# Performance work log

Hardware: AMD Instinct MI355X
Metric: run time of the kernel (lower is better)

The kernel has to match this reference:

```python
import jax, jax.numpy as jnp
import numpy as np

E = 8        # num_experts
TOPK = 2     # k
D = 1024     # input/output size
H = 4096     # expert hidden size


def setup_inputs() -> dict:
    key = jax.random.key(0)
    ks = jax.random.split(key, 8)
    s = 0.02
    return {
        "hidden_states": jax.random.normal(ks[0], (2, 2048, D), dtype=jnp.float32),
        "Wr": jax.random.normal(ks[1], (D, E), dtype=jnp.float32) * s,
        "br": jnp.zeros((E,), dtype=jnp.float32),
        "gate_bias": jnp.zeros((E,), dtype=jnp.float32),
        "W1": jax.random.normal(ks[2], (E, D, H), dtype=jnp.float32) * s,
        "b1": jnp.zeros((E, H), dtype=jnp.float32),
        "W2": jax.random.normal(ks[3], (E, H, D), dtype=jnp.float32) * s,
        "b2": jnp.zeros((E, D), dtype=jnp.float32),
    }


def reference(hidden_states, Wr, br, gate_bias, W1, b1, W2, b2):
    B, S, Din = hidden_states.shape
    x = hidden_states.reshape(B * S, Din)              # [T, D]
    # Router: logits + gate bias, top-k, softmax over the k selected logits
    logits = x @ Wr + br + gate_bias                   # [T, E]
    top_v, top_i = jax.lax.top_k(logits, TOPK)         # [T, k]
    probs = jax.nn.softmax(top_v, axis=-1)             # [T, k]
    # Scatter top-k probs into dense per-expert gate weights [T, E]
    gate = jnp.einsum("tk,tke->te", probs,
                      jax.nn.one_hot(top_i, E, dtype=probs.dtype))
    # Per-expert MLP (exact gelu, eval mode -> no dropout/noise),
    # weighted-combine; zero gate weight == token not routed to expert.
    out = jnp.zeros((B * S, W2.shape[-1]), dtype=x.dtype)
    for e in range(E):
        h = jax.nn.gelu(x @ W1[e] + b1[e], approximate=False)  # [T, H]
        y = h @ W2[e] + b2[e]                                  # [T, D]
        out = out + gate[:, e:e + 1] * y
    return out.reshape(B, S, -1)
```

## Files before the change

kernel.cpp:

```cpp
#include <hip/hip_runtime.h>
#include <hip/hip_bf16.h>
#include <stdint.h>
#include <stddef.h>


#define T_TOK 4096
#define DIM   1024
#define HID   4096
#define NE    8

typedef unsigned short u16;
typedef __bf16 bf16x8 __attribute__((ext_vector_type(8)));
typedef float  f32x4  __attribute__((ext_vector_type(4)));
typedef u16    u16x8  __attribute__((ext_vector_type(8)));

__device__ __forceinline__ u16 f2bf(float f) {
  union { float f; uint32_t u; } v; v.f = f;
  uint32_t u = v.u;
  return (u16)((u + 0x7fffu + ((u >> 16) & 1u)) >> 16);
}

__device__ __forceinline__ void async_load16(const void* g, void* l) {
  typedef __attribute__((address_space(1))) void GPtr;
  typedef __attribute__((address_space(3))) void LPtr;
  __builtin_amdgcn_global_load_lds((GPtr*)g, (LPtr*)l, 16, 0, 0);
}

__global__ void router_kernel(const float* __restrict__ x, const float* __restrict__ Wr,
                              const float* __restrict__ br, const float* __restrict__ gb,
                              int* __restrict__ counts, int* __restrict__ lists,
                              float* __restrict__ gate_p) {
  const int t = blockIdx.x * 4 + (threadIdx.x >> 6);
  const int lane = threadIdx.x & 63;
  const float* xr = x + (size_t)t * DIM;
  float acc[NE];
#pragma unroll
  for (int e = 0; e < NE; ++e) acc[e] = 0.f;
#pragma unroll
  for (int i = 0; i < DIM / 64; ++i) {
    const int k = i * 64 + lane;
    const float xv = xr[k];
    const float4 w0 = *reinterpret_cast<const float4*>(Wr + (size_t)k * NE);
    const float4 w1 = *reinterpret_cast<const float4*>(Wr + (size_t)k * NE + 4);
    acc[0] += xv * w0.x; acc[1] += xv * w0.y; acc[2] += xv * w0.z; acc[3] += xv * w0.w;
    acc[4] += xv * w1.x; acc[5] += xv * w1.y; acc[6] += xv * w1.z; acc[7] += xv * w1.w;
  }
#pragma unroll
  for (int off = 32; off >= 1; off >>= 1) {
#pragma unroll
    for (int e = 0; e < NE; ++e) acc[e] += __shfl_xor(acc[e], off);
  }
  if (lane == 0) {
    float lg[NE];
#pragma unroll
    for (int e = 0; e < NE; ++e) lg[e] = acc[e] + br[e] + gb[e];
    int i0 = 0;
#pragma unroll
    for (int e = 1; e < NE; ++e) if (lg[e] > lg[i0]) i0 = e;
    int i1 = (i0 == 0) ? 1 : 0;
#pragma unroll
    for (int e = 0; e < NE; ++e) if (e != i0 && lg[e] > lg[i1]) i1 = e;
    const float ev = expf(lg[i1] - lg[i0]);
    const float p0 = 1.f / (1.f + ev);
    const float p1 = ev / (1.f + ev);
    const int pos0 = atomicAdd(&counts[i0], 1);
    lists[i0 * T_TOK + pos0] = t * 2 + 0;
    const int pos1 = atomicAdd(&counts[i1], 1);
    lists[i1 * T_TOK + pos1] = t * 2 + 1;
    gate_p[t * 2 + 0] = p0;
    gate_p[t * 2 + 1] = p1;
  }
}

__global__ void cvt_x_kernel(const float* __restrict__ in, u16* __restrict__ out, int n8) {
  const int i = blockIdx.x * blockDim.x + threadIdx.x;
  if (i >= n8) return;
  const float4 a = reinterpret_cast<const float4*>(in)[2 * i];
  const float4 b = reinterpret_cast<const float4*>(in)[2 * i + 1];
  u16x8 r;
  r[0] = f2bf(a.x); r[1] = f2bf(a.y); r[2] = f2bf(a.z); r[3] = f2bf(a.w);
  r[4] = f2bf(b.x); r[5] = f2bf(b.y); r[6] = f2bf(b.z); r[7] = f2bf(b.w);
  *reinterpret_cast<u16x8*>(out + (size_t)i * 8) = r;
}

__global__ void cvt_w_kernel(const float* __restrict__ in, u16* __restrict__ out,
                             int K, int N) {
  __shared__ float tile[64][65];
  const int e = blockIdx.z;
  const int n0 = blockIdx.x * 64, k0 = blockIdx.y * 64;
  const int tid = threadIdx.x;
  const float* src = in + (size_t)e * K * N;
#pragma unroll
  for (int r = 0; r < 16; ++r) {
    const int kr = r * 4 + (tid >> 6);
    tile[kr][tid & 63] = src[(size_t)(k0 + kr) * N + n0 + (tid & 63)];
  }
  __syncthreads();
  u16* dst = out + (size_t)e * N * K;
#pragma unroll
  for (int r = 0; r < 8; ++r) {
    const int nr = r * 8 + (tid >> 5);
    const int kc = (tid & 31) * 2;
    ushort2 v;
    v.x = f2bf(tile[kc][nr]);
    v.y = f2bf(tile[kc + 1][nr]);
    *reinterpret_cast<ushort2*>(&dst[(size_t)(n0 + nr) * K + k0 + kc]) = v;
  }
}

template <int KT, int NT, int PHASE>
__global__ __launch_bounds__(256, 2)
void gemm_kernel(const u16* __restrict__ Abase, const u16* __restrict__ Bt,
                 const float* __restrict__ bias, const int* __restrict__ counts,
                 const int* __restrict__ lists, const float* __restrict__ gate_p,
                 u16* __restrict__ hout, float* __restrict__ yout) {
  const int e = blockIdx.z;
  const int cnt = counts[e];
  const int m0 = blockIdx.y * 128;
  if (m0 >= cnt) return;
  const int n0 = blockIdx.x * 128;
  const int tid = threadIdx.x;
  const int lane = tid & 63, wid = tid >> 6;
  const int wr = wid >> 1, wc = wid & 1;

  __shared__ alignas(16) u16 As[128 * 72];
  __shared__ alignas(16) u16 Bs[128 * 64];
  __shared__ int rowp[128];

  if (tid < 128) {
    const int idx = m0 + tid;
    rowp[tid] = lists[e * T_TOK + (idx < cnt ? idx : cnt - 1)];
  }
  __syncthreads();

  const u16* aptr[4];
#pragma unroll
  for (int i = 0; i < 4; ++i) {
    const int r = i * 32 + (tid >> 3);
    const int p = rowp[r];
    const int arow = (PHASE == 1) ? (p >> 1) : p;
    aptr[i] = Abase + (size_t)arow * KT + (tid & 7) * 8;
  }
  const u16* bsrc = Bt + ((size_t)e * NT + n0) * KT;

  f32x4 acc[4][4];
#pragma unroll
  for (int a = 0; a < 4; ++a)
#pragma unroll
    for (int b = 0; b < 4; ++b) acc[a][b] = f32x4{0.f, 0.f, 0.f, 0.f};

  for (int k0 = 0; k0 < KT; k0 += 64) {
#pragma unroll
    for (int j = 0; j < 4; ++j) {
      const int brow = j * 32 + wid * 8;
      const u16* src = bsrc + (size_t)(brow + (lane >> 3)) * KT + k0 + (lane & 7) * 8;
      async_load16(src, &Bs[brow * 64]);
    }
#pragma unroll
    for (int i = 0; i < 4; ++i) {
      const bf16x8 v = *reinterpret_cast<const bf16x8*>(aptr[i] + k0);
      *reinterpret_cast<bf16x8*>(&As[((size_t)(i * 32 + (tid >> 3))) * 72 + (tid & 7) * 8]) = v;
    }
    __syncthreads();
#pragma unroll
    for (int kk = 0; kk < 2; ++kk) {
      bf16x8 af[4], bfr[4];
#pragma unroll
      for (int fm = 0; fm < 4; ++fm)
        af[fm] = *reinterpret_cast<const bf16x8*>(
            &As[(wr * 64 + fm * 16 + (lane & 15)) * 72 + kk * 32 + (lane >> 4) * 8]);
#pragma unroll
      for (int fn = 0; fn < 4; ++fn)
        bfr[fn] = *reinterpret_cast<const bf16x8*>(
            &Bs[(wc * 64 + fn * 16 + (lane & 15)) * 64 + kk * 32 + (lane >> 4) * 8]);
#pragma unroll
      for (int fm = 0; fm < 4; ++fm)
#pragma unroll
        for (int fn = 0; fn < 4; ++fn)
          acc[fm][fn] = __builtin_amdgcn_mfma_f32_16x16x32_bf16(af[fm], bfr[fn],
                                                                acc[fm][fn], 0, 0, 0);
    }
    __syncthreads();
  }

  const float* bias_e = bias + (size_t)e * NT;
#pragma unroll
  for (int fm = 0; fm < 4; ++fm) {
#pragma unroll
    for (int r = 0; r < 4; ++r) {
      const int row = wr * 64 + fm * 16 + (lane >> 4) * 4 + r;
      if (m0 + row >= cnt) continue;
      const int p = rowp[row];
#pragma unroll
      for (int fn = 0; fn < 4; ++fn) {
        const int n = n0 + wc * 64 + fn * 16 + (lane & 15);
        const float v = acc[fm][fn][r] + bias_e[n];
        if (PHASE == 1) {
          const float g = 0.5f * v * (1.0f + erff(v * 0.70710678118654752f));
          hout[(size_t)p * NT + n] = f2bf(g);
        } else if (PHASE == 2) {
          yout[(size_t)p * NT + n] = gate_p[p] * v;
        } else {
          atomicAdd(&yout[(size_t)(p >> 1) * NT + n], gate_p[p] * v);
        }
      }
    }
  }
}

__global__ void combine_kernel(const float* __restrict__ yp, float* __restrict__ out) {
  const int i = blockIdx.x * blockDim.x + threadIdx.x;
  const int t = i >> 8;
  const int d4 = i & 255;
  const float4 a = reinterpret_cast<const float4*>(yp)[(size_t)(2 * t) * 256 + d4];
  const float4 b = reinterpret_cast<const float4*>(yp)[(size_t)(2 * t) * 256 + 256 + d4];
  float4 o; o.x = a.x + b.x; o.y = a.y + b.y; o.z = a.z + b.z; o.w = a.w + b.w;
  reinterpret_cast<float4*>(out)[i] = o;
}

extern "C" void kernel_launch(void* const* d_in, const int* in_sizes, int n_in,
                              void* d_out, int out_size, void* d_ws, size_t ws_size,
                              hipStream_t stream) {
  const float* x  = (const float*)d_in[0];
  const float* Wr = (const float*)d_in[1];
  const float* br = (const float*)d_in[2];
  const float* gb = (const float*)d_in[3];
  const float* W1 = (const float*)d_in[4];
  const float* b1 = (const float*)d_in[5];
  const float* W2 = (const float*)d_in[6];
  const float* b2 = (const float*)d_in[7];
  float* out = (float*)d_out;

  char* ws = (char*)d_ws;
  size_t off = 0;
  int*   counts = (int*)(ws + off);   off += 256;
  int*   lists  = (int*)(ws + off);   off += (size_t)NE * T_TOK * 4;
  float* gate_p = (float*)(ws + off); off += (size_t)T_TOK * 2 * 4;
  u16*   xb     = (u16*)(ws + off);   off += (size_t)T_TOK * DIM * 2;
  u16*   wbuf   = (u16*)(ws + off);   off += (size_t)NE * DIM * HID * 2;
  u16*   hbuf   = (u16*)(ws + off);   off += (size_t)T_TOK * 2 * HID * 2;
  const size_t need_base = off;
  float* ypair  = (float*)(ws + off);
  const size_t need_full = off + (size_t)T_TOK * 2 * DIM * 4;
  const bool use_ypair = (ws_size >= need_full);
  (void)need_base;

  hipMemsetAsync(counts, 0, 32, stream);
  router_kernel<<<T_TOK / 4, 256, 0, stream>>>(x, Wr, br, gb, counts, lists, gate_p);
  cvt_x_kernel<<<(T_TOK * DIM / 8 + 255) / 256, 256, 0, stream>>>(x, xb, T_TOK * DIM / 8);
  cvt_w_kernel<<<dim3(HID / 64, DIM / 64, NE), 256, 0, stream>>>(W1, wbuf, DIM, HID);
  gemm_kernel<DIM, HID, 1><<<dim3(HID / 128, T_TOK / 128, NE), 256, 0, stream>>>(
      xb, wbuf, b1, counts, lists, gate_p, hbuf, nullptr);
  cvt_w_kernel<<<dim3(DIM / 64, HID / 64, NE), 256, 0, stream>>>(W2, wbuf, HID, DIM);
  if (use_ypair) {
    gemm_kernel<HID, DIM, 2><<<dim3(DIM / 128, T_TOK / 128, NE), 256, 0, stream>>>(
        hbuf, wbuf, b2, counts, lists, gate_p, nullptr, ypair);
    combine_kernel<<<T_TOK, 256, 0, stream>>>(ypair, out);
  } else {
    hipMemsetAsync(out, 0, (size_t)out_size * 4, stream);
    gemm_kernel<HID, DIM, 3><<<dim3(DIM / 128, T_TOK / 128, NE), 256, 0, stream>>>(
        hbuf, wbuf, b2, counts, lists, gate_p, nullptr, out);
  }
}
```

Measured before the change: 476.6 us.

## Double-buffer GEMM LDS tiles with prefetch and XOR-swizzle B layout

The expert GEMM kernel now keeps two LDS buffers for the A and B tiles. While MFMAs run on the current tile, it prefetches the next K tile: A goes through registers and B through async global-to-LDS loads. This needs one barrier per step instead of two. B tiles are also stored with an XOR swizzle of their 16-byte slots to cut LDS bank conflicts on the fragment reads. The cost is doubled LDS use (about 69KB per block), which may limit occupancy against the launch bound of 2 blocks per CU, plus extra register pressure from the prefetch.

```diff
diff --git a/kernel.cpp b/kernel.cpp
--- a/kernel.cpp
+++ b/kernel.cpp
@@ -123,8 +123,8 @@
   const int lane = tid & 63, wid = tid >> 6;
   const int wr = wid >> 1, wc = wid & 1;
 
-  __shared__ alignas(16) u16 As[128 * 72];
-  __shared__ alignas(16) u16 Bs[128 * 64];
+  __shared__ alignas(16) u16 As[2][128 * 72];
+  __shared__ alignas(16) u16 Bs[2][128 * 64];
   __shared__ int rowp[128];
 
   if (tid < 128) {
@@ -142,6 +142,8 @@
     aptr[i] = Abase + (size_t)arow * KT + (tid & 7) * 8;
   }
   const u16* bsrc = Bt + ((size_t)e * NT + n0) * KT;
+  const int brow_lane = lane >> 3;
+  const int bslot = (lane & 7) ^ brow_lane;
 
   f32x4 acc[4][4];
 #pragma unroll
@@ -149,39 +151,73 @@
 #pragma unroll
     for (int b = 0; b < 4; ++b) acc[a][b] = f32x4{0.f, 0.f, 0.f, 0.f};
 
-  for (int k0 = 0; k0 < KT; k0 += 64) {
-#pragma unroll
-    for (int j = 0; j < 4; ++j) {
-      const int brow = j * 32 + wid * 8;
-      const u16* src = bsrc + (size_t)(brow + (lane >> 3)) * KT + k0 + (lane & 7) * 8;
-      async_load16(src, &Bs[brow * 64]);
-    }
-#pragma unroll
-    for (int i = 0; i < 4; ++i) {
-      const bf16x8 v = *reinterpret_cast<const bf16x8*>(aptr[i] + k0);
-      *reinterpret_cast<bf16x8*>(&As[((size_t)(i * 32 + (tid >> 3))) * 72 + (tid & 7) * 8]) = v;
-    }
-    __syncthreads();
-#pragma unroll
-    for (int kk = 0; kk < 2; ++kk) {
-      bf16x8 af[4], bfr[4];
-#pragma unroll
-      for (int fm = 0; fm < 4; ++fm)
-        af[fm] = *reinterpret_cast<const bf16x8*>(
-            &As[(wr * 64 + fm * 16 + (lane & 15)) * 72 + kk * 32 + (lane >> 4) * 8]);
-#pragma unroll
-      for (int fn = 0; fn < 4; ++fn)
-        bfr[fn] = *reinterpret_cast<const bf16x8*>(
-            &Bs[(wc * 64 + fn * 16 + (lane & 15)) * 64 + kk * 32 + (lane >> 4) * 8]);
-#pragma unroll
-      for (int fm = 0; fm < 4; ++fm)
-#pragma unroll
-        for (int fn = 0; fn < 4; ++fn)
-          acc[fm][fn] = __builtin_amdgcn_mfma_f32_16x16x32_bf16(af[fm], bfr[fn],
-                                                                acc[fm][fn], 0, 0, 0);
-    }
-    __syncthreads();
-  }
+  constexpr int nkt = KT / 64;
+  bf16x8 areg[4];
+
+#pragma unroll
+  for (int i = 0; i < 4; ++i) areg[i] = *reinterpret_cast<const bf16x8*>(aptr[i]);
+#pragma unroll
+  for (int j = 0; j < 4; ++j) {
+    const int brow = j * 32 + wid * 8;
+    async_load16(bsrc + (size_t)(brow + brow_lane) * KT + bslot * 8, &Bs[0][brow * 64]);
+  }
+#pragma unroll
+  for (int i = 0; i < 4; ++i)
+    *reinterpret_cast<bf16x8*>(&As[0][(i * 32 + (tid >> 3)) * 72 + (tid & 7) * 8]) = areg[i];
+  __syncthreads();
+
+#define GEMM_STEP(CUR, NXT, T)                                                       \
+  {                                                                                  \
+    const int t_ = (T);                                                              \
+    const bool pf_ = (t_ + 1 < nkt);                                                 \
+    if (pf_) {                                                                       \
+      _Pragma("unroll")                                                              \
+      for (int i = 0; i < 4; ++i)                                                    \
+        areg[i] = *reinterpret_cast<const bf16x8*>(aptr[i] + (t_ + 1) * 64);         \
+      _Pragma("unroll")                                                              \
+      for (int j = 0; j < 4; ++j) {                                                  \
+        const int brow = j * 32 + wid * 8;                                           \
+        async_load16(bsrc + (size_t)(brow + brow_lane) * KT + (t_ + 1) * 64 +        \
+                         bslot * 8,                                                  \
+                     &Bs[NXT][brow * 64]);                                           \
+      }                                                                              \
+    }                                                                                \
+    _Pragma("unroll")                                                                \
+    for (int kk = 0; kk < 2; ++kk) {                                                 \
+      bf16x8 af[4], bfr[4];                                                          \
+      _Pragma("unroll")                                                              \
+      for (int fm = 0; fm < 4; ++fm)                                                 \
+        af[fm] = *reinterpret_cast<const bf16x8*>(                                   \
+            &As[CUR][(wr * 64 + fm * 16 + (lane & 15)) * 72 + kk * 32 +              \
+                     (lane >> 4) * 8]);                                              \
+      _Pragma("unroll")                                                              \
+      for (int fn = 0; fn < 4; ++fn) {                                               \
+        const int r2 = wc * 64 + fn * 16 + (lane & 15);                              \
+        const int ls = kk * 4 + (lane >> 4);                                         \
+        bfr[fn] = *reinterpret_cast<const bf16x8*>(                                  \
+            &Bs[CUR][r2 * 64 + ((ls ^ (r2 & 7)) * 8)]);                              \
+      }                                                                              \
+      _Pragma("unroll")                                                              \
+      for (int fm = 0; fm < 4; ++fm)                                                 \
+        _Pragma("unroll")                                                            \
+        for (int fn = 0; fn < 4; ++fn)                                               \
+          acc[fm][fn] = __builtin_amdgcn_mfma_f32_16x16x32_bf16(af[fm], bfr[fn],     \
+                                                                acc[fm][fn], 0, 0, 0); \
+    }                                                                                \
+    if (pf_) {                                                                       \
+      _Pragma("unroll")                                                              \
+      for (int i = 0; i < 4; ++i)                                                    \
+        *reinterpret_cast<bf16x8*>(                                                  \
+            &As[NXT][(i * 32 + (tid >> 3)) * 72 + (tid & 7) * 8]) = areg[i];         \
+    }                                                                                \
+    __syncthreads();                                                                 \
+  }
+
+  for (int t = 0; t < nkt; t += 2) {
+    GEMM_STEP(0, 1, t);
+    GEMM_STEP(1, 0, t + 1);
+  }
+#undef GEMM_STEP
 
   const float* bias_e = bias + (size_t)e * NT;
 #pragma unroll
@@ -239,11 +275,9 @@
   u16*   xb     = (u16*)(ws + off);   off += (size_t)T_TOK * DIM * 2;
   u16*   wbuf   = (u16*)(ws + off);   off += (size_t)NE * DIM * HID * 2;
   u16*   hbuf   = (u16*)(ws + off);   off += (size_t)T_TOK * 2 * HID * 2;
-  const size_t need_base = off;
   float* ypair  = (float*)(ws + off);
   const size_t need_full = off + (size_t)T_TOK * 2 * DIM * 4;
   const bool use_ypair = (ws_size >= need_full);
-  (void)need_base;
 
   hipMemsetAsync(counts, 0, 32, stream);
   router_kernel<<<T_TOK / 4, 256, 0, stream>>>(x, Wr, br, gb, counts, lists, gate_p);
```

Result: slower. 496.6 us (+4.2%).

## Rework expert GEMM into 256x128 tiles with triple-buffered async LDS pipeline

Applied to the files above, without the earlier changes.

Rewrites the grouped expert GEMM to use 512-thread blocks computing 256x128 output tiles, with both A (gathered token rows) and B loaded via async global-to-LDS copies into a three-stage ring buffer with XOR-swizzled layout. MFMA work is split into two halves per K step, with prefetch of stage t+2 issued between them and s_setprio raised around MFMA bursts. This aims to hide global-load latency and LDS bank conflicts and raise arithmetic intensity per block. It uses 144KB of LDS per block, which limits occupancy, and relies on hand-placed waitcnt and barriers being correct.

```diff
diff --git a/kernel.cpp b/kernel.cpp
--- a/kernel.cpp
+++ b/kernel.cpp
@@ -109,92 +109,160 @@
 }
 
 template <int KT, int NT, int PHASE>
-__global__ __launch_bounds__(256, 2)
+__global__ __launch_bounds__(512, 2)
 void gemm_kernel(const u16* __restrict__ Abase, const u16* __restrict__ Bt,
                  const float* __restrict__ bias, const int* __restrict__ counts,
                  const int* __restrict__ lists, const float* __restrict__ gate_p,
                  u16* __restrict__ hout, float* __restrict__ yout) {
   const int e = blockIdx.z;
   const int cnt = counts[e];
-  const int m0 = blockIdx.y * 128;
+  const int m0 = blockIdx.y * 256;
   if (m0 >= cnt) return;
   const int n0 = blockIdx.x * 128;
   const int tid = threadIdx.x;
-  const int lane = tid & 63, wid = tid >> 6;
-  const int wr = wid >> 1, wc = wid & 1;
-
-  __shared__ alignas(16) u16 As[128 * 72];
-  __shared__ alignas(16) u16 Bs[128 * 64];
-  __shared__ int rowp[128];
-
-  if (tid < 128) {
+  const int lane = tid & 63, w = tid >> 6;
+  const int wm = w >> 2, wn = w & 3;
+
+  __shared__ alignas(16) u16 lds[73728];
+  __shared__ int rowp[256];
+
+  if (tid < 256) {
     const int idx = m0 + tid;
     rowp[tid] = lists[e * T_TOK + (idx < cnt ? idx : cnt - 1)];
   }
   __syncthreads();
 
-  const u16* aptr[4];
+  const int srow = w * 8 + (lane >> 3);
+  const int sslot = (lane & 7) ^ (lane >> 3);
+  const u16* aP[4];
 #pragma unroll
   for (int i = 0; i < 4; ++i) {
-    const int r = i * 32 + (tid >> 3);
-    const int p = rowp[r];
+    const int p = rowp[i * 64 + srow];
     const int arow = (PHASE == 1) ? (p >> 1) : p;
-    aptr[i] = Abase + (size_t)arow * KT + (tid & 7) * 8;
-  }
-  const u16* bsrc = Bt + ((size_t)e * NT + n0) * KT;
-
-  f32x4 acc[4][4];
-#pragma unroll
-  for (int a = 0; a < 4; ++a)
-#pragma unroll
-    for (int b = 0; b < 4; ++b) acc[a][b] = f32x4{0.f, 0.f, 0.f, 0.f};
-
-  for (int k0 = 0; k0 < KT; k0 += 64) {
-#pragma unroll
-    for (int j = 0; j < 4; ++j) {
-      const int brow = j * 32 + wid * 8;
-      const u16* src = bsrc + (size_t)(brow + (lane >> 3)) * KT + k0 + (lane & 7) * 8;
-      async_load16(src, &Bs[brow * 64]);
+    aP[i] = Abase + (size_t)arow * KT + sslot * 8;
+  }
+  const u16* bP[2];
+#pragma unroll
+  for (int i = 0; i < 2; ++i)
+    bP[i] = Bt + ((size_t)e * NT + n0 + i * 64 + srow) * KT + sslot * 8;
+
+  constexpr int nkt = KT / 64;
+
+#define STAGE(TT, BB)                                                          \
+  {                                                                            \
+    _Pragma("unroll")                                                          \
+    for (int i = 0; i < 4; ++i)                                                \
+      async_load16(aP[i] + (TT) * 64, &lds[(BB) * 16384 + (i * 64 + w * 8) * 64]); \
+    _Pragma("unroll")                                                          \
+    for (int i = 0; i < 2; ++i)                                                \
+      async_load16(bP[i] + (TT) * 64,                                          \
+                   &lds[49152 + (BB) * 8192 + (i * 64 + w * 8) * 64]);         \
+  }
+
+  f32x4 acc[8][2];
+#pragma unroll
+  for (int a = 0; a < 8; ++a)
+#pragma unroll
+    for (int b = 0; b < 2; ++b) acc[a][b] = f32x4{0.f, 0.f, 0.f, 0.f};
+
+  STAGE(0, 0);
+  STAGE(1, 1);
+  asm volatile("s_waitcnt vmcnt(6)" ::: "memory");
+  __builtin_amdgcn_sched_barrier(0);
+  __builtin_amdgcn_s_barrier();
+
+  int cur = 0;
+  const int l15 = lane & 15, lks = lane >> 4;
+  for (int t = 0; t < nkt; ++t) {
+    const int abase = cur * 16384;
+    const int bbase = 49152 + cur * 8192;
+    bf16x8 bf[2][2];
+    {
+      bf16x8 af[4][2];
+#pragma unroll
+      for (int fm = 0; fm < 4; ++fm) {
+        const int r = wm * 128 + fm * 16 + l15;
+#pragma unroll
+        for (int ks = 0; ks < 2; ++ks) {
+          const int ls = ks * 4 + lks;
+          af[fm][ks] = *reinterpret_cast<const bf16x8*>(
+              &lds[abase + r * 64 + ((ls ^ (r & 7)) * 8)]);
+        }
+      }
+#pragma unroll
+      for (int nf = 0; nf < 2; ++nf) {
+        const int r = wn * 32 + nf * 16 + l15;
+#pragma unroll
+        for (int ks = 0; ks < 2; ++ks) {
+          const int ls = ks * 4 + lks;
+          bf[nf][ks] = *reinterpret_cast<const bf16x8*>(
+              &lds[bbase + r * 64 + ((ls ^ (r & 7)) * 8)]);
+        }
+      }
+      if (t + 2 < nkt) {
+        const int nxt2 = (cur == 0) ? 2 : cur - 1;
+        STAGE(t + 2, nxt2);
+      }
+      __builtin_amdgcn_s_barrier();
+      __builtin_amdgcn_s_setprio(1);
+#pragma unroll
+      for (int fm = 0; fm < 4; ++fm)
+#pragma unroll
+        for (int nf = 0; nf < 2; ++nf)
+#pragma unroll
+          for (int ks = 0; ks < 2; ++ks)
+            acc[fm][nf] = __builtin_amdgcn_mfma_f32_16x16x32_bf16(
+                af[fm][ks], bf[nf][ks], acc[fm][nf], 0, 0, 0);
+      __builtin_amdgcn_s_setprio(0);
+      __builtin_amdgcn_s_barrier();
     }
-#pragma unroll
-    for (int i = 0; i < 4; ++i) {
-      const bf16x8 v = *reinterpret_cast<const bf16x8*>(aptr[i] + k0);
-      *reinterpret_cast<bf16x8*>(&As[((size_t)(i * 32 + (tid >> 3))) * 72 + (tid & 7) * 8]) = v;
+    {
+      bf16x8 af[4][2];
+#pragma unroll
+      for (int fm = 0; fm < 4; ++fm) {
+        const int r = wm * 128 + 64 + fm * 16 + l15;
+#pragma unroll
+        for (int ks = 0; ks < 2; ++ks) {
+          const int ls = ks * 4 + lks;
+          af[fm][ks] = *reinterpret_cast<const bf16x8*>(
+              &lds[abase + r * 64 + ((ls ^ (r & 7)) * 8)]);
+        }
+      }
+      if (t < nkt - 2) {
+        asm volatile("s_waitcnt vmcnt(6)" ::: "memory");
+      } else if (t == nkt - 2) {
+        asm volatile("s_waitcnt vmcnt(0)" ::: "memory");
+      }
+      __builtin_amdgcn_sched_barrier(0);
+      __builtin_amdgcn_s_barrier();
+      __builtin_amdgcn_s_setprio(1);
+#pragma unroll
+      for (int fm = 0; fm < 4; ++fm)
+#pragma unroll
+        for (int nf = 0; nf < 2; ++nf)
+#pragma unroll
+          for (int ks = 0; ks < 2; ++ks)
+            acc[4 + fm][nf] = __builtin_amdgcn_mfma_f32_16x16x32_bf16(
+                af[fm][ks], bf[nf][ks], acc[4 + fm][nf], 0, 0, 0);
+      __builtin_amdgcn_s_setprio(0);
+      __builtin_amdgcn_s_barrier();
     }
-    __syncthreads();
-#pragma unroll
-    for (int kk = 0; kk < 2; ++kk) {
-      bf16x8 af[4], bfr[4];
-#pragma unroll
-      for (int fm = 0; fm < 4; ++fm)
-        af[fm] = *reinterpret_cast<const bf16x8*>(
-            &As[(wr * 64 + fm * 16 + (lane & 15)) * 72 + kk * 32 + (lane >> 4) * 8]);
-#pragma unroll
-      for (int fn = 0; fn < 4; ++fn)
-        bfr[fn] = *reinterpret_cast<const bf16x8*>(
-            &Bs[(wc * 64 + fn * 16 + (lane & 15)) * 64 + kk * 32 + (lane >> 4) * 8]);
-#pragma unroll
-      for (int fm = 0; fm < 4; ++fm)
-#pragma unroll
-        for (int fn = 0; fn < 4; ++fn)
-          acc[fm][fn] = __builtin_amdgcn_mfma_f32_16x16x32_bf16(af[fm], bfr[fn],
-                                                                acc[fm][fn], 0, 0, 0);
-    }
-    __syncthreads();
-  }
+    cur = (cur == 2) ? 0 : cur + 1;
+  }
+#undef STAGE
 
   const float* bias_e = bias + (size_t)e * NT;
 #pragma unroll
-  for (int fm = 0; fm < 4; ++fm) {
+  for (int fm = 0; fm < 8; ++fm) {
 #pragma unroll
     for (int r = 0; r < 4; ++r) {
-      const int row = wr * 64 + fm * 16 + (lane >> 4) * 4 + r;
+      const int row = wm * 128 + ((fm & 4) << 4) + (fm & 3) * 16 + (lane >> 4) * 4 + r;
       if (m0 + row >= cnt) continue;
       const int p = rowp[row];
 #pragma unroll
-      for (int fn = 0; fn < 4; ++fn) {
-        const int n = n0 + wc * 64 + fn * 16 + (lane & 15);
-        const float v = acc[fm][fn][r] + bias_e[n];
+      for (int nf = 0; nf < 2; ++nf) {
+        const int n = n0 + wn * 32 + nf * 16 + (lane & 15);
+        const float v = acc[fm][nf][r] + bias_e[n];
         if (PHASE == 1) {
           const float g = 0.5f * v * (1.0f + erff(v * 0.70710678118654752f));
           hout[(size_t)p * NT + n] = f2bf(g);
@@ -239,26 +307,24 @@
   u16*   xb     = (u16*)(ws + off);   off += (size_t)T_TOK * DIM * 2;
   u16*   wbuf   = (u16*)(ws + off);   off += (size_t)NE * DIM * HID * 2;
   u16*   hbuf   = (u16*)(ws + off);   off += (size_t)T_TOK * 2 * HID * 2;
-  const size_t need_base = off;
   float* ypair  = (float*)(ws + off);
   const size_t need_full = off + (size_t)T_TOK * 2 * DIM * 4;
   const bool use_ypair = (ws_size >= need_full);
-  (void)need_base;
 
   hipMemsetAsync(counts, 0, 32, stream);
   router_kernel<<<T_TOK / 4, 256, 0, stream>>>(x, Wr, br, gb, counts, lists, gate_p);
   cvt_x_kernel<<<(T_TOK * DIM / 8 + 255) / 256, 256, 0, stream>>>(x, xb, T_TOK * DIM / 8);
   cvt_w_kernel<<<dim3(HID / 64, DIM / 64, NE), 256, 0, stream>>>(W1, wbuf, DIM, HID);
-  gemm_kernel<DIM, HID, 1><<<dim3(HID / 128, T_TOK / 128, NE), 256, 0, stream>>>(
+  gemm_kernel<DIM, HID, 1><<<dim3(HID / 128, T_TOK * 2 / 256, NE), 512, 0, stream>>>(
       xb, wbuf, b1, counts, lists, gate_p, hbuf, nullptr);
   cvt_w_kernel<<<dim3(DIM / 64, HID / 64, NE), 256, 0, stream>>>(W2, wbuf, HID, DIM);
   if (use_ypair) {
-    gemm_kernel<HID, DIM, 2><<<dim3(DIM / 128, T_TOK / 128, NE), 256, 0, stream>>>(
+    gemm_kernel<HID, DIM, 2><<<dim3(DIM / 128, T_TOK * 2 / 256, NE), 512, 0, stream>>>(
         hbuf, wbuf, b2, counts, lists, gate_p, nullptr, ypair);
     combine_kernel<<<T_TOK, 256, 0, stream>>>(ypair, out);
   } else {
     hipMemsetAsync(out, 0, (size_t)out_size * 4, stream);
-    gemm_kernel<HID, DIM, 3><<<dim3(DIM / 128, T_TOK / 128, NE), 256, 0, stream>>>(
+    gemm_kernel<HID, DIM, 3><<<dim3(DIM / 128, T_TOK * 2 / 256, NE), 512, 0, stream>>>(
         hbuf, wbuf, b2, counts, lists, gate_p, nullptr, out);
   }
 }
```

After: 563.7 us. 1.18x slower.

## Rewrite MoE GEMM with 256x256 tiles, swizzled LDS pipeline, split-K and tile table

Applied to the files above, without the earlier changes.

The expert GEMM is restructured. It now uses 512-thread blocks computing 256x256 output tiles, XOR-swizzled LDS and a register-staged double buffer. Global loads for the next K step are interleaved with MFMA work across four barrier phases, and MFMA priority is raised. A small tile-table kernel packs only the occupied (expert, row-tile) pairs into the grid, replacing the dense expert × max-tile grid with its early exits. The second GEMM is split along K into two partial outputs, which a 4-way combine kernel sums. The aim is more data reuse per LDS load and better overlap of loads with MFMA, at the cost of a large 128KB LDS footprint (low occupancy) and extra partial-sum traffic.

```diff
diff --git a/kernel.cpp b/kernel.cpp
--- a/kernel.cpp
+++ b/kernel.cpp
@@ -8,6 +8,7 @@
 #define DIM   1024
 #define HID   4096
 #define NE    8
+#define MT_MAX 40
 
 typedef unsigned short u16;
 typedef __bf16 bf16x8 __attribute__((ext_vector_type(8)));
@@ -18,12 +19,6 @@
   union { float f; uint32_t u; } v; v.f = f;
   uint32_t u = v.u;
   return (u16)((u + 0x7fffu + ((u >> 16) & 1u)) >> 16);
-}
-
-__device__ __forceinline__ void async_load16(const void* g, void* l) {
-  typedef __attribute__((address_space(1))) void GPtr;
-  typedef __attribute__((address_space(3))) void LPtr;
-  __builtin_amdgcn_global_load_lds((GPtr*)g, (LPtr*)l, 16, 0, 0);
 }
 
 __global__ void router_kernel(const float* __restrict__ x, const float* __restrict__ Wr,
@@ -72,6 +67,20 @@
   }
 }
 
+__global__ void tile_table_kernel(const int* __restrict__ counts, int* __restrict__ tab) {
+  if (threadIdx.x == 0) {
+    int tot = 0;
+    for (int e = 0; e < NE; ++e) {
+      const int c = counts[e];
+      const int nt = (c + 255) >> 8;
+      for (int i = 0; i < nt && tot < MT_MAX; ++i) {
+        tab[tot * 2] = e; tab[tot * 2 + 1] = i * 256; ++tot;
+      }
+    }
+    for (; tot < MT_MAX; ++tot) tab[tot * 2] = -1;
+  }
+}
+
 __global__ void cvt_x_kernel(const float* __restrict__ in, u16* __restrict__ out, int n8) {
   const int i = blockIdx.x * blockDim.x + threadIdx.x;
   if (i >= n8) return;
@@ -108,113 +117,209 @@
   }
 }
 
-template <int KT, int NT, int PHASE>
-__global__ __launch_bounds__(256, 2)
+__device__ __forceinline__ void ld_afrags(const u16* sm, int cA, int fmh, int wm,
+                                          int l15, int swz0, int swz1, bf16x8 af[4][2]) {
+#pragma unroll
+  for (int f = 0; f < 4; ++f) {
+    const int r = fmh * 128 + wm * 64 + f * 16 + l15;
+    af[f][0] = *reinterpret_cast<const bf16x8*>(&sm[cA + r * 64 + swz0 * 8]);
+    af[f][1] = *reinterpret_cast<const bf16x8*>(&sm[cA + r * 64 + swz1 * 8]);
+  }
+}
+__device__ __forceinline__ void ld_bfrags(const u16* sm, int cA, int nfh, int wn,
+                                          int l15, int swz0, int swz1, bf16x8 bfr[2][2]) {
+#pragma unroll
+  for (int g = 0; g < 2; ++g) {
+    const int r = nfh * 128 + wn * 32 + g * 16 + l15;
+    bfr[g][0] = *reinterpret_cast<const bf16x8*>(&sm[32768 + cA + r * 64 + swz0 * 8]);
+    bfr[g][1] = *reinterpret_cast<const bf16x8*>(&sm[32768 + cA + r * 64 + swz1 * 8]);
+  }
+}
+__device__ __forceinline__ void wr_half(u16* sm, int baseoff, int h, int trow, int wslot,
+                                        const bf16x8 v[2]) {
+#pragma unroll
+  for (int j = 0; j < 2; ++j) {
+    const int r = h * 128 + j * 64 + trow;
+    *reinterpret_cast<bf16x8*>(&sm[baseoff + r * 64 + wslot * 8]) = v[j];
+  }
+}
+
+#define PH_SYNC()                                           \
+  asm volatile("s_waitcnt lgkmcnt(0)" ::: "memory");        \
+  __builtin_amdgcn_s_barrier();                             \
+  __builtin_amdgcn_sched_barrier(0);
+
+#define MMQ(FMH, NFH, AF, BF)                                                   \
+  __builtin_amdgcn_s_setprio(1);                                                \
+  _Pragma("unroll") for (int f_ = 0; f_ < 4; ++f_)                              \
+  _Pragma("unroll") for (int g_ = 0; g_ < 2; ++g_)                              \
+  _Pragma("unroll") for (int ks_ = 0; ks_ < 2; ++ks_)                           \
+    acc[(FMH) * 4 + f_][(NFH) * 2 + g_] =                                       \
+        __builtin_amdgcn_mfma_f32_16x16x32_bf16(                                \
+            AF[f_][ks_], BF[g_][ks_], acc[(FMH) * 4 + f_][(NFH) * 2 + g_],      \
+            0, 0, 0);                                                           \
+  __builtin_amdgcn_s_setprio(0);
+
+template <int KT, int NT, int NSPLIT, int PHASE>
+__global__ __launch_bounds__(512, 2)
 void gemm_kernel(const u16* __restrict__ Abase, const u16* __restrict__ Bt,
                  const float* __restrict__ bias, const int* __restrict__ counts,
                  const int* __restrict__ lists, const float* __restrict__ gate_p,
+                 const int* __restrict__ tab,
                  u16* __restrict__ hout, float* __restrict__ yout) {
-  const int e = blockIdx.z;
+  const int e = tab[blockIdx.x * 2];
+  if (e < 0) return;
+  const int m0 = tab[blockIdx.x * 2 + 1];
   const int cnt = counts[e];
-  const int m0 = blockIdx.y * 128;
-  if (m0 >= cnt) return;
-  const int n0 = blockIdx.x * 128;
+  const int n0 = blockIdx.y * 256;
+  const int z = blockIdx.z;
+  const int kbase = z * (KT / NSPLIT);
+  constexpr int nkt = (KT / NSPLIT) / 64;
+
   const int tid = threadIdx.x;
-  const int lane = tid & 63, wid = tid >> 6;
-  const int wr = wid >> 1, wc = wid & 1;
-
-  __shared__ alignas(16) u16 As[128 * 72];
-  __shared__ alignas(16) u16 Bs[128 * 64];
-  __shared__ int rowp[128];
-
-  if (tid < 128) {
+  const int lane = tid & 63, w = tid >> 6;
+  const int wm = w >> 2, wn = w & 3;
+  const int l15 = lane & 15, lks = lane >> 4;
+  const int rb = l15 & 7;
+  const int swz0 = lks ^ rb, swz1 = (4 + lks) ^ rb;
+
+  __shared__ alignas(16) u16 lds[65536];
+  __shared__ int rowp[256];
+
+  if (tid < 256) {
     const int idx = m0 + tid;
     rowp[tid] = lists[e * T_TOK + (idx < cnt ? idx : cnt - 1)];
   }
   __syncthreads();
 
-  const u16* aptr[4];
-#pragma unroll
-  for (int i = 0; i < 4; ++i) {
-    const int r = i * 32 + (tid >> 3);
-    const int p = rowp[r];
-    const int arow = (PHASE == 1) ? (p >> 1) : p;
-    aptr[i] = Abase + (size_t)arow * KT + (tid & 7) * 8;
-  }
-  const u16* bsrc = Bt + ((size_t)e * NT + n0) * KT;
-
-  f32x4 acc[4][4];
-#pragma unroll
-  for (int a = 0; a < 4; ++a)
+  const int trow = tid >> 3;
+  const int tslot = tid & 7;
+  const int wslot = tslot ^ (trow & 7);
+  const u16* aP[2][2];
+  const u16* bP[2][2];
+#pragma unroll
+  for (int h = 0; h < 2; ++h)
+#pragma unroll
+    for (int j = 0; j < 2; ++j) {
+      const int r = h * 128 + j * 64 + trow;
+      const int p = rowp[r];
+      const int arow = (PHASE == 1) ? (p >> 1) : p;
+      aP[h][j] = Abase + (size_t)arow * KT + kbase + tslot * 8;
+      bP[h][j] = Bt + ((size_t)e * NT + n0 + r) * KT + kbase + tslot * 8;
+    }
+
+  f32x4 acc[8][4];
+#pragma unroll
+  for (int a = 0; a < 8; ++a)
 #pragma unroll
     for (int b = 0; b < 4; ++b) acc[a][b] = f32x4{0.f, 0.f, 0.f, 0.f};
 
-  for (int k0 = 0; k0 < KT; k0 += 64) {
-#pragma unroll
-    for (int j = 0; j < 4; ++j) {
-      const int brow = j * 32 + wid * 8;
-      const u16* src = bsrc + (size_t)(brow + (lane >> 3)) * KT + k0 + (lane & 7) * 8;
-      async_load16(src, &Bs[brow * 64]);
+  bf16x8 aL0[2], aL1[2], bL0[2], bL1[2], af[4][2], bfr[2][2];
+
+  {
+    bf16x8 w0[2], w1[2];
+#pragma unroll
+    for (int j = 0; j < 2; ++j) {
+      w0[j]  = *reinterpret_cast<const bf16x8*>(aP[0][j]);
+      w1[j]  = *reinterpret_cast<const bf16x8*>(bP[0][j]);
+      aL1[j] = *reinterpret_cast<const bf16x8*>(aP[1][j]);
+      bL1[j] = *reinterpret_cast<const bf16x8*>(bP[1][j]);
     }
-#pragma unroll
-    for (int i = 0; i < 4; ++i) {
-      const bf16x8 v = *reinterpret_cast<const bf16x8*>(aptr[i] + k0);
-      *reinterpret_cast<bf16x8*>(&As[((size_t)(i * 32 + (tid >> 3))) * 72 + (tid & 7) * 8]) = v;
-    }
-    __syncthreads();
-#pragma unroll
-    for (int kk = 0; kk < 2; ++kk) {
-      bf16x8 af[4], bfr[4];
-#pragma unroll
-      for (int fm = 0; fm < 4; ++fm)
-        af[fm] = *reinterpret_cast<const bf16x8*>(
-            &As[(wr * 64 + fm * 16 + (lane & 15)) * 72 + kk * 32 + (lane >> 4) * 8]);
-#pragma unroll
-      for (int fn = 0; fn < 4; ++fn)
-        bfr[fn] = *reinterpret_cast<const bf16x8*>(
-            &Bs[(wc * 64 + fn * 16 + (lane & 15)) * 64 + kk * 32 + (lane >> 4) * 8]);
-#pragma unroll
-      for (int fm = 0; fm < 4; ++fm)
-#pragma unroll
-        for (int fn = 0; fn < 4; ++fn)
-          acc[fm][fn] = __builtin_amdgcn_mfma_f32_16x16x32_bf16(af[fm], bfr[fn],
-                                                                acc[fm][fn], 0, 0, 0);
-    }
-    __syncthreads();
-  }
+    wr_half(lds, 0, 0, trow, wslot, w0);
+    wr_half(lds, 32768, 0, trow, wslot, w1);
+  }
+
+#define TILE(C, T)                                                                   \
+  {                                                                                  \
+    constexpr int cA = (C) * 16384;                                                  \
+    constexpr int nA = ((C) ^ 1) * 16384;                                            \
+    const int tn = (T) + 1;                                                          \
+                                       \
+    PH_SYNC();                                                                       \
+    ld_afrags(lds, cA, 0, wm, l15, swz0, swz1, af);                                  \
+    ld_bfrags(lds, cA, 0, wn, l15, swz0, swz1, bfr);                                 \
+    if (tn < nkt) {                                                                  \
+      aL0[0] = *reinterpret_cast<const bf16x8*>(aP[0][0] + tn * 64);                 \
+      aL0[1] = *reinterpret_cast<const bf16x8*>(aP[0][1] + tn * 64);                 \
+    }                                                                                \
+    wr_half(lds, 32768 + cA, 1, trow, wslot, bL1);                                   \
+    MMQ(0, 0, af, bfr);                                                              \
+                                          \
+    PH_SYNC();                                                                       \
+    ld_bfrags(lds, cA, 1, wn, l15, swz0, swz1, bfr);                                 \
+    if (tn < nkt) {                                                                  \
+      bL0[0] = *reinterpret_cast<const bf16x8*>(bP[0][0] + tn * 64);                 \
+      bL0[1] = *reinterpret_cast<const bf16x8*>(bP[0][1] + tn * 64);                 \
+    }                                                                                \
+    wr_half(lds, cA, 1, trow, wslot, aL1);                                           \
+    MMQ(0, 1, af, bfr);                                                              \
+                                      \
+    PH_SYNC();                                                                       \
+    ld_afrags(lds, cA, 1, wm, l15, swz0, swz1, af);                                  \
+    ld_bfrags(lds, cA, 0, wn, l15, swz0, swz1, bfr);                                 \
+    if (tn < nkt) {                                                                  \
+      bL1[0] = *reinterpret_cast<const bf16x8*>(bP[1][0] + tn * 64);                 \
+      bL1[1] = *reinterpret_cast<const bf16x8*>(bP[1][1] + tn * 64);                 \
+    }                                                                                \
+    wr_half(lds, nA, 0, trow, wslot, aL0);                                           \
+    MMQ(1, 0, af, bfr);                                                              \
+                            \
+    ld_bfrags(lds, cA, 1, wn, l15, swz0, swz1, bfr);                                 \
+    if (tn < nkt) {                                                                  \
+      aL1[0] = *reinterpret_cast<const bf16x8*>(aP[1][0] + tn * 64);                 \
+      aL1[1] = *reinterpret_cast<const bf16x8*>(aP[1][1] + tn * 64);                 \
+    }                                                                                \
+    wr_half(lds, 32768 + nA, 0, trow, wslot, bL0);                                   \
+    MMQ(1, 1, af, bfr);                                                              \
+  }
+
+  for (int t = 0; t < nkt; t += 2) {
+    TILE(0, t);
+    TILE(1, t + 1);
+  }
+#undef TILE
 
   const float* bias_e = bias + (size_t)e * NT;
-#pragma unroll
-  for (int fm = 0; fm < 4; ++fm) {
+  const float bz = (z == 0) ? 1.f : 0.f;
+#pragma unroll
+  for (int fm = 0; fm < 8; ++fm) {
+    const int rbase = (fm >> 2) * 128 + wm * 64 + (fm & 3) * 16 + (lane >> 4) * 4;
 #pragma unroll
     for (int r = 0; r < 4; ++r) {
-      const int row = wr * 64 + fm * 16 + (lane >> 4) * 4 + r;
+      const int row = rbase + r;
       if (m0 + row >= cnt) continue;
       const int p = rowp[row];
 #pragma unroll
-      for (int fn = 0; fn < 4; ++fn) {
-        const int n = n0 + wc * 64 + fn * 16 + (lane & 15);
-        const float v = acc[fm][fn][r] + bias_e[n];
+      for (int nf = 0; nf < 4; ++nf) {
+        const int n = n0 + (nf >> 1) * 128 + wn * 32 + (nf & 1) * 16 + l15;
+        const float v = acc[fm][nf][r];
         if (PHASE == 1) {
-          const float g = 0.5f * v * (1.0f + erff(v * 0.70710678118654752f));
+          const float vb = v + bias_e[n];
+          const float g = 0.5f * vb * (1.0f + erff(vb * 0.70710678118654752f));
           hout[(size_t)p * NT + n] = f2bf(g);
         } else if (PHASE == 2) {
-          yout[(size_t)p * NT + n] = gate_p[p] * v;
+          yout[(size_t)z * T_TOK * 2 * NT + (size_t)p * NT + n] =
+              gate_p[p] * (v + bz * bias_e[n]);
         } else {
-          atomicAdd(&yout[(size_t)(p >> 1) * NT + n], gate_p[p] * v);
+          atomicAdd(&yout[(size_t)(p >> 1) * NT + n], gate_p[p] * (v + bz * bias_e[n]));
         }
       }
     }
   }
 }
 
-__global__ void combine_kernel(const float* __restrict__ yp, float* __restrict__ out) {
+__global__ void combine4_kernel(const float* __restrict__ yp, float* __restrict__ out) {
   const int i = blockIdx.x * blockDim.x + threadIdx.x;
-  const int t = i >> 8;
-  const int d4 = i & 255;
-  const float4 a = reinterpret_cast<const float4*>(yp)[(size_t)(2 * t) * 256 + d4];
-  const float4 b = reinterpret_cast<const float4*>(yp)[(size_t)(2 * t) * 256 + 256 + d4];
-  float4 o; o.x = a.x + b.x; o.y = a.y + b.y; o.z = a.z + b.z; o.w = a.w + b.w;
+  const int t = i >> 8, d4 = i & 255;
+  const size_t r0 = (size_t)(2 * t) * 256 + d4;
+  const size_t zoff = (size_t)T_TOK * 2 * DIM / 4;
+  const float4 a = reinterpret_cast<const float4*>(yp)[r0];
+  const float4 b = reinterpret_cast<const float4*>(yp)[r0 + 256];
+  const float4 c = reinterpret_cast<const float4*>(yp)[zoff + r0];
+  const float4 d = reinterpret_cast<const float4*>(yp)[zoff + r0 + 256];
+  float4 o;
+  o.x = a.x + b.x + c.x + d.x; o.y = a.y + b.y + c.y + d.y;
+  o.z = a.z + b.z + c.z + d.z; o.w = a.w + b.w + c.w + d.w;
   reinterpret_cast<float4*>(out)[i] = o;
 }
 
@@ -234,31 +339,31 @@
   char* ws = (char*)d_ws;
   size_t off = 0;
   int*   counts = (int*)(ws + off);   off += 256;
+  int*   ttab   = (int*)(ws + off);   off += 512;
   int*   lists  = (int*)(ws + off);   off += (size_t)NE * T_TOK * 4;
   float* gate_p = (float*)(ws + off); off += (size_t)T_TOK * 2 * 4;
   u16*   xb     = (u16*)(ws + off);   off += (size_t)T_TOK * DIM * 2;
   u16*   wbuf   = (u16*)(ws + off);   off += (size_t)NE * DIM * HID * 2;
   u16*   hbuf   = (u16*)(ws + off);   off += (size_t)T_TOK * 2 * HID * 2;
-  const size_t need_base = off;
   float* ypair  = (float*)(ws + off);
-  const size_t need_full = off + (size_t)T_TOK * 2 * DIM * 4;
+  const size_t need_full = off + (size_t)2 * T_TOK * 2 * DIM * 4;
   const bool use_ypair = (ws_size >= need_full);
-  (void)need_base;
 
   hipMemsetAsync(counts, 0, 32, stream);
   router_kernel<<<T_TOK / 4, 256, 0, stream>>>(x, Wr, br, gb, counts, lists, gate_p);
+  tile_table_kernel<<<1, 64, 0, stream>>>(counts, ttab);
   cvt_x_kernel<<<(T_TOK * DIM / 8 + 255) / 256, 256, 0, stream>>>(x, xb, T_TOK * DIM / 8);
   cvt_w_kernel<<<dim3(HID / 64, DIM / 64, NE), 256, 0, stream>>>(W1, wbuf, DIM, HID);
-  gemm_kernel<DIM, HID, 1><<<dim3(HID / 128, T_TOK / 128, NE), 256, 0, stream>>>(
-      xb, wbuf, b1, counts, lists, gate_p, hbuf, nullptr);
+  gemm_kernel<DIM, HID, 1, 1><<<dim3(MT_MAX, HID / 256, 1), 512, 0, stream>>>(
+      xb, wbuf, b1, counts, lists, gate_p, ttab, hbuf, nullptr);
   cvt_w_kernel<<<dim3(DIM / 64, HID / 64, NE), 256, 0, stream>>>(W2, wbuf, HID, DIM);
   if (use_ypair) {
-    gemm_kernel<HID, DIM, 2><<<dim3(DIM / 128, T_TOK / 128, NE), 256, 0, stream>>>(
-        hbuf, wbuf, b2, counts, lists, gate_p, nullptr, ypair);
-    combine_kernel<<<T_TOK, 256, 0, stream>>>(ypair, out);
+    gemm_kernel<HID, DIM, 2, 2><<<dim3(MT_MAX, DIM / 256, 2), 512, 0, stream>>>(
+        hbuf, wbuf, b2, counts, lists, gate_p, ttab, nullptr, ypair);
+    combine4_kernel<<<T_TOK * DIM / 4 / 256, 256, 0, stream>>>(ypair, out);
   } else {
     hipMemsetAsync(out, 0, (size_t)out_size * 4, stream);
-    gemm_kernel<HID, DIM, 3><<<dim3(DIM / 128, T_TOK / 128, NE), 256, 0, stream>>>(
-        hbuf, wbuf, b2, counts, lists, gate_p, nullptr, out);
-  }
-}
+    gemm_kernel<HID, DIM, 2, 3><<<dim3(MT_MAX, DIM / 256, 2), 512, 0, stream>>>(
+        hbuf, wbuf, b2, counts, lists, gate_p, ttab, nullptr, out);
+  }
+}
```

After: 500.2 us. 1.05x slower.
